# Kernel tuning notes

Measured on AMD Instinct MI355X. Metric: run time of the kernel, lower is better.

Reference implementation:

```python
import jax, jax.numpy as jnp
import numpy as np

HEADS = 8
DIM_HEAD = 64
NB_FEATURES = 256
CHUNK = 128          # chunk size used by performer's causal_linear_attention_noncuda
EPS_KERNEL = 1e-4    # eps in softmax_kernel feature map
EPS_DENOM = 1e-6     # eps added to k_cumsum in the denominator


def softmax_kernel(data, proj, is_query):
    # FAVOR+ positive softmax random features (performer_pytorch.softmax_kernel)
    # data: [B,H,N,D], proj: [M,D]
    d = data.shape[-1]
    normalizer = d ** -0.25
    ratio = proj.shape[0] ** -0.5
    data_dash = jnp.einsum('bhnd,md->bhnm', data * normalizer, proj)
    # ||x||^2 / (2*sqrt(d))
    diag = jnp.sum(data * data, axis=-1, keepdims=True) * 0.5 * (normalizer ** 2)
    if is_query:
        m = jax.lax.stop_gradient(jnp.max(data_dash, axis=-1, keepdims=True))
    else:
        m = jax.lax.stop_gradient(jnp.max(data_dash, axis=(-1, -2), keepdims=True))
    return ratio * (jnp.exp(data_dash - diag - m) + EPS_KERNEL)


def causal_linear_attention(qp, kp, v, chunk=CHUNK):
    # Chunked causal linear attention (O(N) in seq len):
    # out_i = q'_i . S_i / (q'_i . z_i), S_i = sum_{j<=i} k'_j v_j^T, z_i = cumsum k'_j
    B, H, N, M = qp.shape
    E = v.shape[-1]
    C = N // chunk

    def to_chunks(x):
        return x.reshape(B, H, C, chunk, x.shape[-1]).transpose(2, 0, 1, 3, 4)

    qc, kc, vc = to_chunks(qp), to_chunks(kp), to_chunks(v)
    k0 = jnp.zeros((B, H, M), qp.dtype)
    s0 = jnp.zeros((B, H, M, E), qp.dtype)

    def step(carry, inp):
        k_last, s_last = carry
        q, k, vv = inp  # [B,H,c,M], [B,H,c,M], [B,H,c,E]
        k_cum = k_last[:, :, None, :] + jnp.cumsum(k, axis=2)           # [B,H,c,M]
        d_inv = 1.0 / jnp.einsum('bhnm,bhnm->bhn', q, k_cum + EPS_DENOM)
        ctx = jnp.einsum('bhnm,bhne->bhnme', k, vv)                      # [B,H,c,M,E]
        s_cum = s_last[:, :, None] + jnp.cumsum(ctx, axis=2)             # [B,H,c,M,E]
        out = jnp.einsum('bhnme,bhnm,bhn->bhne', s_cum, q, d_inv)        # [B,H,c,E]
        return (k_cum[:, :, -1, :], s_cum[:, :, -1]), out

    _, outs = jax.lax.scan(step, (k0, s0), (qc, kc, vc))  # [C,B,H,c,E]
    return outs.transpose(1, 2, 0, 3, 4).reshape(B, H, N, E)


def setup_inputs() -> dict:
    key = jax.random.key(0)
    k1, k2, k3, k4 = jax.random.split(key, 4)
    B, N, D = 4, 2048, 512
    return {
        'query': jax.random.normal(k1, (B, N, D), jnp.float32),
        'key': jax.random.normal(k2, (B, N, D), jnp.float32),
        'value': jax.random.normal(k3, (B, N, D), jnp.float32),
        'projection': jax.random.normal(k4, (NB_FEATURES, DIM_HEAD), jnp.float32),
    }


def reference(query, key, value, projection):
    B, N, D = query.shape

    def split(x):  # [B,N,D] -> [B,H,N,Dh]
        return x.reshape(B, N, HEADS, DIM_HEAD).transpose(0, 2, 1, 3)

    q, k, v = split(query), split(key), split(value)
    qp = softmax_kernel(q, projection, is_query=True)
    kp = softmax_kernel(k, projection, is_query=False)
    out = causal_linear_attention(qp, kp, v)
    return out.transpose(0, 2, 1, 3).reshape(B, N, D)
```

## Files before the change

kernel.cpp:

```cpp
#include <hip/hip_runtime.h>
#include <math.h>

#define BB 4
#define NN 2048
#define DD 512
#define HH 8
#define DH 64
#define MM 256
#define BH 32
#define CHK 128
#define NCH 16
#define ROWS (BH*NN)

constexpr float NRM   = 0.35355339059327373f;
constexpr float RATIO = 0.0625f;
constexpr float EPSK  = 1e-4f;
constexpr float EPSD  = 1e-6f;
constexpr float REPS  = 0.0625f * 1e-4f;

#define OFFB_QP   ((size_t)0)
#define OFFB_SP   ((size_t)33554432)
#define OFFB_KP   (OFFB_SP + (size_t)16777216)
#define OFFB_VT   (OFFB_KP + (size_t)33554432)
#define OFFB_Z    (OFFB_VT + (size_t)8388608)
#define OFFB_KMP  (OFFB_Z  + (size_t)524288)

typedef __attribute__((ext_vector_type(8))) short short8;
typedef __attribute__((ext_vector_type(4))) float f32x4;

__device__ __forceinline__ float b2f(ushort u) {
  union { float f; unsigned int i; } x; x.i = ((unsigned int)u) << 16; return x.f;
}
__device__ __forceinline__ ushort f2b(float f) {
  unsigned int u = __float_as_uint(f);
  unsigned int r = (u + 0x7FFFu + ((u >> 16) & 1u)) >> 16;
  return (ushort)r;
}

#define MFMA(a,b,c) __builtin_amdgcn_mfma_f32_16x16x32_bf16(a, b, c, 0, 0, 0)

template<int MODE>
__device__ __forceinline__ void featm_body(const float* __restrict__ inp,
                                           const float* __restrict__ proj,
                                           char* __restrict__ ws,
                                           char* lds, int blk) {
  ushort* xh = (ushort*)lds;
  ushort* xl = xh + 64*72;
  ushort* qt = (ushort*)lds;
  float* diag_s = (float*)(lds + 33792);
  float (*wmax)[4] = (float(*)[4])(lds + 34048);
  float* kred = (float*)(lds + 35072);

  const int t  = threadIdx.x;
  const int w  = t >> 6;
  const int l  = t & 63;
  const int lq = l >> 4;
  const int ln = l & 15;

  const int rowbase = blk * 64;
  const int bh = rowbase >> 11;
  const int b  = bh >> 3, h = bh & 7;
  const int n0 = rowbase & (NN - 1);

  {
    const int r  = t >> 2;
    const int c0 = (t & 3) * 16;
    const float* src = inp + ((size_t)(b*NN + n0 + r))*DD + h*DH + c0;
    float vv[16];
    #pragma unroll
    for (int j = 0; j < 4; ++j) {
      float4 v = *(const float4*)(src + j*4);
      vv[4*j+0] = v.x*NRM; vv[4*j+1] = v.y*NRM;
      vv[4*j+2] = v.z*NRM; vv[4*j+3] = v.w*NRM;
    }
    float s = 0.f;
    ushort hi[16], lo[16];
    #pragma unroll
    for (int j = 0; j < 16; ++j) {
      s += vv[j]*vv[j];
      hi[j] = f2b(vv[j]);
      lo[j] = f2b(vv[j] - b2f(hi[j]));
    }
    *(short8*)(xh + r*72 + c0)     = *(short8*)&hi[0];
    *(short8*)(xh + r*72 + c0 + 8) = *(short8*)&hi[8];
    *(short8*)(xl + r*72 + c0)     = *(short8*)&lo[0];
    *(short8*)(xl + r*72 + c0 + 8) = *(short8*)&lo[8];
    s += __shfl_xor(s, 1); s += __shfl_xor(s, 2);
    if ((t & 3) == 0) diag_s[r] = 0.5f * s;
  }

  short8 bfr[2][2][2];
  #pragma unroll
  for (int p = 0; p < 2; ++p)
    #pragma unroll
    for (int ntl = 0; ntl < 2; ++ntl) {
      const float* pr = proj + (size_t)(p*128 + w*32 + ntl*16 + ln)*DH;
      #pragma unroll
      for (int kk = 0; kk < 2; ++kk) {
        float4 f0 = *(const float4*)(pr + kk*32 + lq*8);
        float4 f1 = *(const float4*)(pr + kk*32 + lq*8 + 4);
        ushort u[8] = {f2b(f0.x), f2b(f0.y), f2b(f0.z), f2b(f0.w),
                       f2b(f1.x), f2b(f1.y), f2b(f1.z), f2b(f1.w)};
        bfr[p][ntl][kk] = *(short8*)&u[0];
      }
    }

  f32x4 acc[4][4];
  #pragma unroll
  for (int mt = 0; mt < 4; ++mt)
    #pragma unroll
    for (int c = 0; c < 4; ++c) acc[mt][c] = (f32x4){0.f,0.f,0.f,0.f};

  __syncthreads();

  #pragma unroll
  for (int kk = 0; kk < 2; ++kk) {
    short8 ah[4], al[4];
    #pragma unroll
    for (int mt = 0; mt < 4; ++mt) {
      ah[mt] = *(const short8*)(xh + (mt*16 + ln)*72 + kk*32 + lq*8);
      al[mt] = *(const short8*)(xl + (mt*16 + ln)*72 + kk*32 + lq*8);
    }
    #pragma unroll
    for (int p = 0; p < 2; ++p)
      #pragma unroll
      for (int ntl = 0; ntl < 2; ++ntl) {
        short8 bf = bfr[p][ntl][kk];
        #pragma unroll
        for (int mt = 0; mt < 4; ++mt) {
          acc[mt][2*p+ntl] = MFMA(al[mt], bf, acc[mt][2*p+ntl]);
          acc[mt][2*p+ntl] = MFMA(ah[mt], bf, acc[mt][2*p+ntl]);
        }
      }
  }

  if (MODE == 0) {
    #pragma unroll
    for (int mt = 0; mt < 4; ++mt)
      #pragma unroll
      for (int reg = 0; reg < 4; ++reg) {
        float m = acc[mt][0][reg];
        #pragma unroll
        for (int c = 1; c < 4; ++c) m = fmaxf(m, acc[mt][c][reg]);
        m = fmaxf(m, __shfl_xor(m, 1));
        m = fmaxf(m, __shfl_xor(m, 2));
        m = fmaxf(m, __shfl_xor(m, 4));
        m = fmaxf(m, __shfl_xor(m, 8));
        if (ln == 0) wmax[mt*16 + lq*4 + reg][w] = m;
      }
  } else {
    float mx = -1e30f;
    #pragma unroll
    for (int mt = 0; mt < 4; ++mt)
      #pragma unroll
      for (int c = 0; c < 4; ++c)
        #pragma unroll
        for (int reg = 0; reg < 4; ++reg) mx = fmaxf(mx, acc[mt][c][reg]);
    #pragma unroll
    for (int m = 1; m < 64; m <<= 1) mx = fmaxf(mx, __shfl_xor(mx, m));
    if (l == 0) kred[w] = mx;
  }
  __syncthreads();

  float km = 0.f;
  if (MODE == 1) {
    km = fmaxf(fmaxf(kred[0], kred[1]), fmaxf(kred[2], kred[3]));
    if (t == 0) ((float*)(ws + OFFB_KMP))[blk] = km;
  }

  #pragma unroll
  for (int mt = 0; mt < 4; ++mt)
    #pragma unroll
    for (int reg = 0; reg < 4; ++reg) {
      const int row = mt*16 + lq*4 + reg;
      float rm;
      if (MODE == 0) {
        float4 wm4 = *(const float4*)&wmax[row][0];
        rm = fmaxf(fmaxf(wm4.x, wm4.y), fmaxf(wm4.z, wm4.w));
      } else {
        rm = km;
      }
      const float dg = diag_s[row];
      #pragma unroll
      for (int c = 0; c < 4; ++c) {
        const int f = (c >> 1)*128 + w*32 + (c & 1)*16 + ln;
        const float e = __expf(acc[mt][c][reg] - dg - rm);
        qt[row*264 + f] = f2b(MODE == 0 ? RATIO*(e + EPSK) : e);
      }
    }
  __syncthreads();

  ushort* dstbase = (ushort*)(ws + (MODE == 0 ? OFFB_QP : OFFB_KP)) + (size_t)rowbase*MM;
  #pragma unroll
  for (int ld = 0; ld < 8; ++ld) {
    int flat = t + 256*ld;
    int row = flat >> 5, g = flat & 31;
    *(short8*)(dstbase + (size_t)row*MM + g*8) = *(const short8*)(qt + row*264 + g*8);
  }
}

__device__ __forceinline__ void vt_body(const float* __restrict__ value,
                                        char* __restrict__ ws,
                                        char* lds, int blk) {
  float (*vsh)[68] = (float(*)[68])lds;
  const int t = threadIdx.x;
  const int bh = blk >> 4, nc = blk & 15;
  const int b = bh >> 3, h = bh & 7;
  const int n0 = nc * CHK;
  #pragma unroll
  for (int l = 0; l < 8; ++l) {
    int flat = t + 256*l;
    int r = flat >> 4, g = flat & 15;
    *(float4*)&vsh[r][g*4] = *(const float4*)(value + ((size_t)(b*NN + n0 + r))*DD + h*DH + g*4);
  }
  __syncthreads();
  const int e = t & 63, qd = t >> 6;
  ushort* vt = (ushort*)(ws + OFFB_VT) + ((size_t)bh*DH + e)*NN + n0 + qd*32;
  #pragma unroll
  for (int p = 0; p < 16; ++p) {
    unsigned int lo = f2b(vsh[qd*32 + 2*p][e]);
    unsigned int hi = f2b(vsh[qd*32 + 2*p + 1][e]);
    ((unsigned int*)vt)[p] = lo | (hi << 16);
  }
}

__global__ __launch_bounds__(256) void mega_kernel(const float* __restrict__ q,
                                                   const float* __restrict__ k,
                                                   const float* __restrict__ v,
                                                   const float* __restrict__ proj,
                                                   char* __restrict__ ws) {
  __shared__ __align__(16) char lds[35088];
  const int blk = blockIdx.x;
  if (blk < 1024)       featm_body<0>(q, proj, ws, lds, blk);
  else if (blk < 2048)  featm_body<1>(k, proj, ws, lds, blk - 1024);
  else                  vt_body(v, ws, lds, blk - 2048);
}

__global__ __launch_bounds__(256) void sprefix_kernel(char* __restrict__ ws) {
  __shared__ __align__(16) unsigned int kpTu[2][16*68];
  __shared__ __align__(16) ushort Vts[2][64*136];
  __shared__ float zred[2][16][16];

  const int t  = threadIdx.x;
  const int w  = t >> 6;
  const int l  = t & 63;
  const int lq = l >> 4;
  const int ln = l & 15;
  const int n  = blockIdx.x;
  const int k8 = n >> 3;
  const int bh = (n & 7) + 8*(k8 >> 4);
  const int ms = k8 & 15;

  const ushort* kpb = (const ushort*)(ws + OFFB_KP) + (size_t)bh*NN*MM + ms*16;
  ushort*       kpw = (ushort*)(ws + OFFB_KP) + (size_t)bh*NN*MM + ms*16;
  const ushort* vtb = (const ushort*)(ws + OFFB_VT) + (size_t)bh*DH*NN;
  ushort* spb = (ushort*)(ws + OFFB_SP) + (size_t)bh*NCH*DH*MM + ms*16;
  float*  zb  = (float*)(ws + OFFB_Z) + (size_t)bh*NCH*MM + ms*16;

  const float* kmp = (const float*)(ws + OFFB_KMP) + bh*32;
  float km = kmp[0];
  #pragma unroll
  for (int i = 1; i < 32; ++i) km = fmaxf(km, kmp[i]);

  const int jp = t >> 1, mo = t & 1;
  const int ve = t >> 4, vg = t & 15;

  short8 ka, kc, vr0, vr1, vr2, vr3;
  if (t < 128) {
    ka = *(const short8*)(kpb + (size_t)(2*jp)*MM + mo*8);
    kc = *(const short8*)(kpb + (size_t)(2*jp+1)*MM + mo*8);
  }
  vr0 = *(const short8*)(vtb + (size_t)(ve     )*NN + vg*8);
  vr1 = *(const short8*)(vtb + (size_t)(ve + 16)*NN + vg*8);
  vr2 = *(const short8*)(vtb + (size_t)(ve + 32)*NN + vg*8);
  vr3 = *(const short8*)(vtb + (size_t)(ve + 48)*NN + vg*8);

  f32x4 acc = (f32x4){0.f,0.f,0.f,0.f};
  float zrun = 0.f;

  for (int tc = 0; tc < NCH; ++tc) {
    const int cur = tc & 1;

    if (t < 128) {
      const float s0 = RATIO * __expf(kmp[tc*2 + w] - km);
      ushort ua[8], uc[8];
      #pragma unroll
      for (int i = 0; i < 8; ++i) {
        ua[i] = f2b(fmaf(b2f((ushort)ka[i]), s0, REPS));
        uc[i] = f2b(fmaf(b2f((ushort)kc[i]), s0, REPS));
      }
      #pragma unroll
      for (int i = 0; i < 8; ++i)
        kpTu[cur][(mo*8 + i)*68 + jp] = (unsigned int)ua[i] | ((unsigned int)uc[i] << 16);
      ushort* kwr = kpw + (size_t)tc*CHK*MM + (size_t)(2*jp)*MM + mo*8;
      *(short8*)kwr        = *(short8*)&ua[0];
      *(short8*)(kwr + MM) = *(short8*)&uc[0];
    }
    {
      ushort* vb = &Vts[cur][0];
      *(short8*)(vb + (ve     )*136 + vg*8) = vr0;
      *(short8*)(vb + (ve + 16)*136 + vg*8) = vr1;
      *(short8*)(vb + (ve + 32)*136 + vg*8) = vr2;
      *(short8*)(vb + (ve + 48)*136 + vg*8) = vr3;
    }
    __syncthreads();

    if (tc + 1 < NCH) {
      const ushort* ksn = kpb + (size_t)(tc+1)*CHK*MM;
      if (t < 128) {
        ka = *(const short8*)(ksn + (size_t)(2*jp)*MM + mo*8);
        kc = *(const short8*)(ksn + (size_t)(2*jp+1)*MM + mo*8);
      }
      const ushort* vtn = vtb + (size_t)(tc+1)*CHK;
      vr0 = *(const short8*)(vtn + (size_t)(ve     )*NN + vg*8);
      vr1 = *(const short8*)(vtn + (size_t)(ve + 16)*NN + vg*8);
      vr2 = *(const short8*)(vtn + (size_t)(ve + 32)*NN + vg*8);
      vr3 = *(const short8*)(vtn + (size_t)(ve + 48)*NN + vg*8);
    }

    if (t < 16) {
      if (tc > 0) {
        float s = 0.f;
        #pragma unroll
        for (int q = 0; q < 16; ++q) s += zred[cur^1][q][t];
        zrun += s;
      }
      zb[(size_t)tc*MM + t] = zrun;
    }
    {
      ushort* sp = spb + (size_t)tc*DH*MM;
      #pragma unroll
      for (int reg = 0; reg < 4; ++reg)
        sp[(size_t)(w*16 + lq*4 + reg)*MM + ln] = f2b(acc[reg]);
    }

    {
      int m = t & 15, q = t >> 4;
      float s = 0.f;
      #pragma unroll
      for (int u = 0; u < 4; ++u) {
        unsigned int p = kpTu[cur][m*68 + q*4 + u];
        s += b2f((ushort)(p & 0xFFFF)) + b2f((ushort)(p >> 16));
      }
      zred[cur][q][m] = s;
    }

    #pragma unroll
    for (int kk = 0; kk < 4; ++kk) {
      short8 af = *(const short8*)(&Vts[cur][0] + (w*16 + ln)*136 + kk*32 + lq*8);
      short8 bf = *(const short8*)((const ushort*)&kpTu[cur][0] + (size_t)ln*136 + kk*32 + lq*8);
      acc = MFMA(af, bf, acc);
    }
  }
}

__global__ __launch_bounds__(256) void fused_kernel(float* __restrict__ out,
                                                    char* __restrict__ ws) {
  __shared__ __align__(16) char lds[52224];
  __shared__ float den_i[128];
  __shared__ float dinv_s[128];

  const int t  = threadIdx.x;
  const int w  = t >> 6;
  const int l  = t & 63;
  const int lq = l >> 4;
  const int ln = l & 15;
  const int rt0 = w;
  const int rt1 = 7 - w;
  const int blk = blockIdx.x;
  const int bh = blk >> 4, tc = blk & 15;
  const int b = bh >> 3, h = bh & 7;
  const size_t rowbase = (size_t)bh*NN + tc*CHK;

  const ushort* qpg = (const ushort*)(ws + OFFB_QP) + rowbase*MM;
  const ushort* kpg = (const ushort*)(ws + OFFB_KP) + rowbase*MM;
  const ushort* spg = (const ushort*)(ws + OFFB_SP) + (size_t)blk*DH*MM;

  ushort* qs = (ushort*)lds;
  ushort* ks = qs + 128*72;
  ushort* ss = ks + 128*72;

  f32x4 acc[2][8];
  #pragma unroll
  for (int mt = 0; mt < 2; ++mt)
    #pragma unroll
    for (int nt = 0; nt < 8; ++nt) acc[mt][nt] = (f32x4){0.f,0.f,0.f,0.f};
  f32x4 oacc[2][4];
  #pragma unroll
  for (int mt = 0; mt < 2; ++mt)
    #pragma unroll
    for (int nt = 0; nt < 4; ++nt) oacc[mt][nt] = (f32x4){0.f,0.f,0.f,0.f};

  for (int mc = 0; mc < 4; ++mc) {
    __syncthreads();
    #pragma unroll
    for (int ld2 = 0; ld2 < 4; ++ld2) {
      int flat = t + 256*ld2; int r = flat >> 3, g = flat & 7;
      *(short8*)(qs + r*72 + g*8) = *(const short8*)(qpg + (size_t)r*MM + mc*64 + g*8);
    }
    #pragma unroll
    for (int ld2 = 0; ld2 < 4; ++ld2) {
      int flat = t + 256*ld2; int r = flat >> 3, g = flat & 7;
      *(short8*)(ks + r*72 + g*8) = *(const short8*)(kpg + (size_t)r*MM + mc*64 + g*8);
    }
    #pragma unroll
    for (int ld2 = 0; ld2 < 2; ++ld2) {
      int flat = t + 256*ld2; int e = flat >> 3, g = flat & 7;
      *(short8*)(ss + e*72 + g*8) = *(const short8*)(spg + (size_t)e*MM + mc*64 + g*8);
    }
    __syncthreads();
    #pragma unroll
    for (int kk = 0; kk < 2; ++kk) {
      short8 af0 = *(const short8*)(qs + (rt0*16 + ln)*72 + kk*32 + lq*8);
      short8 af1 = *(const short8*)(qs + (rt1*16 + ln)*72 + kk*32 + lq*8);
      #pragma unroll
      for (int nt = 0; nt < 8; ++nt) {
        if (nt <= rt1) {
          short8 bf = *(const short8*)(ks + (nt*16 + ln)*72 + kk*32 + lq*8);
          if (nt <= rt0) acc[0][nt] = MFMA(af0, bf, acc[0][nt]);
          acc[1][nt] = MFMA(af1, bf, acc[1][nt]);
        }
      }
      #pragma unroll
      for (int nt = 0; nt < 4; ++nt) {
        short8 bf = *(const short8*)(ss + (nt*16 + ln)*72 + kk*32 + lq*8);
        oacc[0][nt] = MFMA(af0, bf, oacc[0][nt]);
        oacc[1][nt] = MFMA(af1, bf, oacc[1][nt]);
      }
    }
  }

  __syncthreads();

  ushort* P   = (ushort*)lds;
  ushort* Vts = (ushort*)(lds + 34816);

  float rs[2][4] = {{0,0,0,0},{0,0,0,0}};
  #pragma unroll
  for (int mt = 0; mt < 2; ++mt) {
    const int ibase = (mt ? rt1 : rt0) * 16;
    #pragma unroll
    for (int nt = 0; nt < 8; ++nt)
      #pragma unroll
      for (int reg = 0; reg < 4; ++reg) {
        int i = ibase + lq*4 + reg;
        int j = nt*16 + ln;
        float v = (j <= i) ? acc[mt][nt][reg] : 0.f;
        rs[mt][reg] += v;
        P[i*136 + j] = f2b(v);
      }
  }
  #pragma unroll
  for (int mt = 0; mt < 2; ++mt) {
    const int ibase = (mt ? rt1 : rt0) * 16;
    #pragma unroll
    for (int reg = 0; reg < 4; ++reg) {
      float s = rs[mt][reg];
      s += __shfl_xor(s, 1); s += __shfl_xor(s, 2);
      s += __shfl_xor(s, 4); s += __shfl_xor(s, 8);
      if (ln == 0) den_i[ibase + lq*4 + reg] = s;
    }
  }

  const ushort* vtg = (const ushort*)(ws + OFFB_VT) + (size_t)bh*DH*NN + tc*CHK;
  #pragma unroll
  for (int ld2 = 0; ld2 < 4; ++ld2) {
    int flat = t + 256*ld2; int e = flat >> 4, g = flat & 15;
    *(short8*)(Vts + e*136 + g*8) = *(const short8*)(vtg + (size_t)e*NN + g*8);
  }
  __syncthreads();

  {
    const float* zp = (const float*)(ws + OFFB_Z) + (size_t)blk*MM;
    const int r = t >> 1, hf = t & 1;
    const ushort* qrow = qpg + (size_t)r*MM + hf*128;
    float s = 0.f;
    #pragma unroll
    for (int g = 0; g < 16; ++g) {
      short8 qv = *(const short8*)(qrow + g*8);
      const float* zz = zp + hf*128 + g*8;
      #pragma unroll
      for (int x = 0; x < 8; ++x)
        s += b2f((ushort)qv[x]) * (zz[x] + EPSD);
    }
    s += __shfl_xor(s, 1);
    if (hf == 0) dinv_s[r] = 1.0f / (s + den_i[r]);
  }
  __syncthreads();

  #pragma unroll
  for (int kk = 0; kk < 4; ++kk) {
    short8 af0 = *(const short8*)(P + (rt0*16 + ln)*136 + kk*32 + lq*8);
    short8 af1 = *(const short8*)(P + (rt1*16 + ln)*136 + kk*32 + lq*8);
    #pragma unroll
    for (int nt = 0; nt < 4; ++nt) {
      short8 bf = *(const short8*)(Vts + (nt*16 + ln)*136 + kk*32 + lq*8);
      oacc[0][nt] = MFMA(af0, bf, oacc[0][nt]);
      oacc[1][nt] = MFMA(af1, bf, oacc[1][nt]);
    }
  }

  #pragma unroll
  for (int mt = 0; mt < 2; ++mt) {
    const int ibase = (mt ? rt1 : rt0) * 16;
    #pragma unroll
    for (int reg = 0; reg < 4; ++reg) {
      const int i = ibase + lq*4 + reg;
      const float di = dinv_s[i];
      float* dst = out + ((size_t)(b*NN) + tc*CHK + i)*DD + h*DH;
      #pragma unroll
      for (int nt = 0; nt < 4; ++nt)
        dst[nt*16 + ln] = oacc[mt][nt][reg] * di;
    }
  }
}

extern "C" void kernel_launch(void* const* d_in, const int* in_sizes, int n_in,
                              void* d_out, int out_size, void* d_ws, size_t ws_size,
                              hipStream_t stream) {
  (void)in_sizes; (void)n_in; (void)out_size; (void)ws_size;
  const float* q    = (const float*)d_in[0];
  const float* k    = (const float*)d_in[1];
  const float* v    = (const float*)d_in[2];
  const float* proj = (const float*)d_in[3];
  float* out = (float*)d_out;
  char*  ws  = (char*)d_ws;

  mega_kernel<<<2560, 256, 0, stream>>>(q, k, v, proj, ws);
  sprefix_kernel<<<512, 256, 0, stream>>>(ws);
  fused_kernel<<<512, 256, 0, stream>>>(out, ws);
}
```

Before: 181.3 us.

## Split serial chunk-state prefix into parallel per-chunk GEMMs plus scan kernel

Replaces the sprefix kernel, which walked all 16 chunks serially per (bh, m-slice) block, with a fully parallel gchunk kernel. Each block computes one chunk's local k'^T v outer-product sum and k' column sums into an fp32 workspace. A separate lightweight scan kernel then does the exclusive prefix over chunks and writes bf16 states and z sums. This exposes more parallelism and removes the serial loop dependency, at the cost of an extra launch and an fp32 round trip through global memory for the per-chunk states.

```diff
diff --git a/kernel.cpp b/kernel.cpp
--- a/kernel.cpp
+++ b/kernel.cpp
@@ -24,6 +24,7 @@
 #define OFFB_VT   (OFFB_KP + (size_t)33554432)
 #define OFFB_Z    (OFFB_VT + (size_t)8388608)
 #define OFFB_KMP  (OFFB_Z  + (size_t)524288)
+#define OFFB_G    (OFFB_KMP + (size_t)4096)
 
 typedef __attribute__((ext_vector_type(8))) short short8;
 typedef __attribute__((ext_vector_type(4))) float f32x4;
@@ -236,121 +237,121 @@
   else                  vt_body(v, ws, lds, blk - 2048);
 }
 
-__global__ __launch_bounds__(256) void sprefix_kernel(char* __restrict__ ws) {
-  __shared__ __align__(16) unsigned int kpTu[2][16*68];
-  __shared__ __align__(16) ushort Vts[2][64*136];
-  __shared__ float zred[2][16][16];
+__global__ __launch_bounds__(256) void gchunk_kernel(char* __restrict__ ws) {
+  __shared__ __align__(16) unsigned int kpTh[128*68];
+  __shared__ __align__(16) ushort Vts[64*136];
 
   const int t  = threadIdx.x;
   const int w  = t >> 6;
   const int l  = t & 63;
   const int lq = l >> 4;
   const int ln = l & 15;
-  const int n  = blockIdx.x;
-  const int k8 = n >> 3;
-  const int bh = (n & 7) + 8*(k8 >> 4);
-  const int ms = k8 & 15;
-
-  const ushort* kpb = (const ushort*)(ws + OFFB_KP) + (size_t)bh*NN*MM + ms*16;
-  ushort*       kpw = (ushort*)(ws + OFFB_KP) + (size_t)bh*NN*MM + ms*16;
-  const ushort* vtb = (const ushort*)(ws + OFFB_VT) + (size_t)bh*DH*NN;
-  ushort* spb = (ushort*)(ws + OFFB_SP) + (size_t)bh*NCH*DH*MM + ms*16;
-  float*  zb  = (float*)(ws + OFFB_Z) + (size_t)bh*NCH*MM + ms*16;
+
+  const int blk = blockIdx.x;
+  const int mh  = blk & 1;
+  const int tc  = (blk >> 1) & 15;
+  const int bh  = blk >> 5;
 
   const float* kmp = (const float*)(ws + OFFB_KMP) + bh*32;
   float km = kmp[0];
   #pragma unroll
   for (int i = 1; i < 32; ++i) km = fmaxf(km, kmp[i]);
 
-  const int jp = t >> 1, mo = t & 1;
-  const int ve = t >> 4, vg = t & 15;
-
-  short8 ka, kc, vr0, vr1, vr2, vr3;
-  if (t < 128) {
-    ka = *(const short8*)(kpb + (size_t)(2*jp)*MM + mo*8);
-    kc = *(const short8*)(kpb + (size_t)(2*jp+1)*MM + mo*8);
-  }
-  vr0 = *(const short8*)(vtb + (size_t)(ve     )*NN + vg*8);
-  vr1 = *(const short8*)(vtb + (size_t)(ve + 16)*NN + vg*8);
-  vr2 = *(const short8*)(vtb + (size_t)(ve + 32)*NN + vg*8);
-  vr3 = *(const short8*)(vtb + (size_t)(ve + 48)*NN + vg*8);
-
-  f32x4 acc = (f32x4){0.f,0.f,0.f,0.f};
-  float zrun = 0.f;
-
-  for (int tc = 0; tc < NCH; ++tc) {
-    const int cur = tc & 1;
-
-    if (t < 128) {
-      const float s0 = RATIO * __expf(kmp[tc*2 + w] - km);
-      ushort ua[8], uc[8];
-      #pragma unroll
-      for (int i = 0; i < 8; ++i) {
-        ua[i] = f2b(fmaf(b2f((ushort)ka[i]), s0, REPS));
-        uc[i] = f2b(fmaf(b2f((ushort)kc[i]), s0, REPS));
-      }
-      #pragma unroll
-      for (int i = 0; i < 8; ++i)
-        kpTu[cur][(mo*8 + i)*68 + jp] = (unsigned int)ua[i] | ((unsigned int)uc[i] << 16);
-      ushort* kwr = kpw + (size_t)tc*CHK*MM + (size_t)(2*jp)*MM + mo*8;
-      *(short8*)kwr        = *(short8*)&ua[0];
-      *(short8*)(kwr + MM) = *(short8*)&uc[0];
-    }
-    {
-      ushort* vb = &Vts[cur][0];
-      *(short8*)(vb + (ve     )*136 + vg*8) = vr0;
-      *(short8*)(vb + (ve + 16)*136 + vg*8) = vr1;
-      *(short8*)(vb + (ve + 32)*136 + vg*8) = vr2;
-      *(short8*)(vb + (ve + 48)*136 + vg*8) = vr3;
-    }
-    __syncthreads();
-
-    if (tc + 1 < NCH) {
-      const ushort* ksn = kpb + (size_t)(tc+1)*CHK*MM;
-      if (t < 128) {
-        ka = *(const short8*)(ksn + (size_t)(2*jp)*MM + mo*8);
-        kc = *(const short8*)(ksn + (size_t)(2*jp+1)*MM + mo*8);
-      }
-      const ushort* vtn = vtb + (size_t)(tc+1)*CHK;
-      vr0 = *(const short8*)(vtn + (size_t)(ve     )*NN + vg*8);
-      vr1 = *(const short8*)(vtn + (size_t)(ve + 16)*NN + vg*8);
-      vr2 = *(const short8*)(vtn + (size_t)(ve + 32)*NN + vg*8);
-      vr3 = *(const short8*)(vtn + (size_t)(ve + 48)*NN + vg*8);
-    }
-
-    if (t < 16) {
-      if (tc > 0) {
-        float s = 0.f;
-        #pragma unroll
-        for (int q = 0; q < 16; ++q) s += zred[cur^1][q][t];
-        zrun += s;
-      }
-      zb[(size_t)tc*MM + t] = zrun;
-    }
-    {
-      ushort* sp = spb + (size_t)tc*DH*MM;
-      #pragma unroll
-      for (int reg = 0; reg < 4; ++reg)
-        sp[(size_t)(w*16 + lq*4 + reg)*MM + ln] = f2b(acc[reg]);
-    }
-
-    {
-      int m = t & 15, q = t >> 4;
-      float s = 0.f;
-      #pragma unroll
-      for (int u = 0; u < 4; ++u) {
-        unsigned int p = kpTu[cur][m*68 + q*4 + u];
-        s += b2f((ushort)(p & 0xFFFF)) + b2f((ushort)(p >> 16));
-      }
-      zred[cur][q][m] = s;
-    }
-
+  ushort* kpc = (ushort*)(ws + OFFB_KP) + ((size_t)bh*NN + (size_t)tc*CHK)*MM + mh*128;
+  const ushort* vtb = (const ushort*)(ws + OFFB_VT) + (size_t)bh*DH*NN + tc*CHK;
+
+  #pragma unroll
+  for (int it = 0; it < 4; ++it) {
+    int flat = t + 256*it;
+    int jp = flat >> 4, mg = flat & 15;
+    const float s0 = RATIO * __expf(kmp[tc*2 + (jp >> 5)] - km);
+    short8 a = *(const short8*)(kpc + (size_t)(2*jp)*MM + mg*8);
+    short8 c = *(const short8*)(kpc + (size_t)(2*jp+1)*MM + mg*8);
+    ushort ua[8], uc[8];
+    #pragma unroll
+    for (int i = 0; i < 8; ++i) {
+      ua[i] = f2b(fmaf(b2f((ushort)a[i]), s0, REPS));
+      uc[i] = f2b(fmaf(b2f((ushort)c[i]), s0, REPS));
+    }
+    #pragma unroll
+    for (int i = 0; i < 8; ++i)
+      kpTh[(mg*8 + i)*68 + jp] = (unsigned int)ua[i] | ((unsigned int)uc[i] << 16);
+    *(short8*)(kpc + (size_t)(2*jp)*MM + mg*8)   = *(short8*)&ua[0];
+    *(short8*)(kpc + (size_t)(2*jp+1)*MM + mg*8) = *(short8*)&uc[0];
+  }
+  #pragma unroll
+  for (int it = 0; it < 4; ++it) {
+    int slot = t + 256*it;
+    int e = slot >> 4, g = slot & 15;
+    *(short8*)(Vts + e*136 + g*8) = *(const short8*)(vtb + (size_t)e*NN + g*8);
+  }
+  __syncthreads();
+
+  {
+    int m = t >> 1, half = t & 1;
+    float s = 0.f;
+    #pragma unroll
+    for (int u = 0; u < 32; ++u) {
+      unsigned int p = kpTh[m*68 + half*32 + u];
+      s += b2f((ushort)(p & 0xFFFF)) + b2f((ushort)(p >> 16));
+    }
+    s += __shfl_xor(s, 1);
+    if (half == 0)
+      ((float*)(ws + OFFB_Z))[((size_t)bh*NCH + tc)*MM + mh*128 + m] = s;
+  }
+
+  f32x4 acc[8];
+  #pragma unroll
+  for (int nt = 0; nt < 8; ++nt) acc[nt] = (f32x4){0.f,0.f,0.f,0.f};
+  short8 af[4];
+  #pragma unroll
+  for (int kk = 0; kk < 4; ++kk)
+    af[kk] = *(const short8*)(Vts + (w*16 + ln)*136 + kk*32 + lq*8);
+  #pragma unroll
+  for (int nt = 0; nt < 8; ++nt)
     #pragma unroll
     for (int kk = 0; kk < 4; ++kk) {
-      short8 af = *(const short8*)(&Vts[cur][0] + (w*16 + ln)*136 + kk*32 + lq*8);
-      short8 bf = *(const short8*)((const ushort*)&kpTu[cur][0] + (size_t)ln*136 + kk*32 + lq*8);
-      acc = MFMA(af, bf, acc);
-    }
+      short8 bf = *(const short8*)((const ushort*)kpTh + (size_t)(nt*16 + ln)*136 + kk*32 + lq*8);
+      acc[nt] = MFMA(af[kk], bf, acc[nt]);
+    }
+
+  float* gb = (float*)(ws + OFFB_G) + ((size_t)bh*NCH + tc)*DH*MM + mh*128;
+  #pragma unroll
+  for (int nt = 0; nt < 8; ++nt)
+    #pragma unroll
+    for (int reg = 0; reg < 4; ++reg)
+      gb[(size_t)(w*16 + lq*4 + reg)*MM + nt*16 + ln] = acc[nt][reg];
+}
+
+__global__ __launch_bounds__(256) void scan_kernel(char* __restrict__ ws) {
+  const int t  = threadIdx.x;
+  const int bh = blockIdx.x / 17;
+  const int sl = blockIdx.x % 17;
+  if (sl < 16) {
+    const int e  = sl*4 + (t >> 6);
+    const int m4 = (t & 63) * 4;
+    const float* gb = (const float*)(ws + OFFB_G) + ((size_t)bh*NCH*DH + e)*MM + m4;
+    ushort*     spb = (ushort*)(ws + OFFB_SP)     + ((size_t)bh*NCH*DH + e)*MM + m4;
+    float4 g[NCH];
+    #pragma unroll
+    for (int tc = 0; tc < NCH; ++tc)
+      g[tc] = *(const float4*)(gb + (size_t)tc*DH*MM);
+    float4 acc = {0.f, 0.f, 0.f, 0.f};
+    #pragma unroll
+    for (int tc = 0; tc < NCH; ++tc) {
+      ushort4 o;
+      o.x = f2b(acc.x); o.y = f2b(acc.y); o.z = f2b(acc.z); o.w = f2b(acc.w);
+      *(ushort4*)(spb + (size_t)tc*DH*MM) = o;
+      acc.x += g[tc].x; acc.y += g[tc].y; acc.z += g[tc].z; acc.w += g[tc].w;
+    }
+  } else {
+    float* zf = (float*)(ws + OFFB_Z) + (size_t)bh*NCH*MM + t;
+    float g[NCH];
+    #pragma unroll
+    for (int tc = 0; tc < NCH; ++tc) g[tc] = zf[(size_t)tc*MM];
+    float acc = 0.f;
+    #pragma unroll
+    for (int tc = 0; tc < NCH; ++tc) { zf[(size_t)tc*MM] = acc; acc += g[tc]; }
   }
 }
 
@@ -527,6 +528,7 @@
   char*  ws  = (char*)d_ws;
 
   mega_kernel<<<2560, 256, 0, stream>>>(q, k, v, proj, ws);
-  sprefix_kernel<<<512, 256, 0, stream>>>(ws);
+  gchunk_kernel<<<1024, 256, 0, stream>>>(ws);
+  scan_kernel<<<544, 256, 0, stream>>>(ws);
   fused_kernel<<<512, 256, 0, stream>>>(out, ws);
 }
```

New measurement: 187.5 us. 3.4% more time.
